# Kernel tuning notes

Hardware: AMD Instinct MI355X
Metric: run time of the kernel (lower is better)

The kernel has to match this reference:

```python
import jax, jax.numpy as jnp
import numpy as np

B, T, F = 16, 1024, 512       # batch, time, input_dim
G, V, D = 2, 320, 128         # num_groups, num_vars, var_dim (quantized_dim // G)
TAU = 2.0                     # max_temp * decay**0 at num_updates=0
EPS = 1e-7


def setup_inputs() -> dict:
    key = jax.random.key(0)
    kx, kw, kc, kg = jax.random.split(key, 4)
    x = jax.random.normal(kx, (B, T, F), dtype=jnp.float32)
    w_proj = jax.random.normal(kw, (G * V, F), dtype=jnp.float32)  # NormalLinear: std=1
    b_proj = jnp.zeros((G * V,), dtype=jnp.float32)
    codebook = jax.random.uniform(kc, (1, G * V, D), dtype=jnp.float32)  # uniform init
    u = jax.random.uniform(kg, (B * T, G, V), dtype=jnp.float32, minval=1e-10, maxval=1.0)
    gumbel = -jnp.log(-jnp.log(u))
    return {"x": x, "w_proj": w_proj, "b_proj": b_proj, "codebook": codebook, "gumbel": gumbel}


def reference(x, w_proj, b_proj, codebook, gumbel):
    bsz, tsz, _ = x.shape
    # projection -> (B, T, G, V)
    logits = (jnp.einsum("btf,nf->btn", x, w_proj) + b_proj).reshape(bsz, tsz, G, V)

    # hard one-hot of argmax (float32), like scatter_
    k = jnp.argmax(logits, axis=-1)
    hard_x = jax.nn.one_hot(k, V, dtype=jnp.float32)  # (B, T, G, V)

    # code perplexity: mean over batch dim only, sum over (T, G)
    hard_probs = hard_x.mean(axis=0)  # (T, G, V)
    code_perplexity = jnp.exp(-jnp.sum(hard_probs * jnp.log(hard_probs + EPS), axis=-1)).sum()

    # prob perplexity: softmax over codes, mean over all tokens, sum over groups
    flat_logits = logits.reshape(bsz * tsz, G, V)
    avg_probs = jax.nn.softmax(flat_logits, axis=-1).mean(axis=0)  # (G, V)
    prob_perplexity = jnp.exp(-jnp.sum(avg_probs * jnp.log(avg_probs + EPS), axis=-1)).sum()

    # gumbel-softmax, hard=True with straight-through estimator (training path)
    y_soft = jax.nn.softmax((flat_logits + gumbel) / TAU, axis=-1)  # (N, G, V)
    idx = jnp.argmax(y_soft, axis=-1)
    y_hard = jax.nn.one_hot(idx, V, dtype=y_soft.dtype)
    y = y_hard + y_soft - jax.lax.stop_gradient(y_soft)  # (N, G, V)

    # broadcast-multiply + sum over codes == grouped gather/matmul against codebook
    cb_gvd = codebook.reshape(G, V, D)
    quantized = jnp.einsum("ngv,gvd->ngd", y, cb_gvd).reshape(bsz, tsz, G * D)
    return quantized, code_perplexity, prob_perplexity
```

## Files before the change

kernel.cpp:

```cpp
#include <hip/hip_runtime.h>
#include <math.h>

#define B_   16
#define T_   1024
#define F_   512
#define G_   2
#define V_   320
#define D_   128
#define N_   (B_ * T_)
#define GV   (G_ * V_)
#define EPS_ 1e-7f

#define ROWS    64
#define THREADS 512
#define NBLK    (N_ / ROWS)
#define CHK     32
#define NCH     (F_ / CHK)
#define NCC     (3 * NCH)

#define BOFF  0
#define AOFF  40960
#define BUFSZ 45056
#define LDSZ  (2 * BUFSZ)

typedef _Float16 half8 __attribute__((ext_vector_type(8)));
typedef _Float16 half4 __attribute__((ext_vector_type(4)));
typedef float f32x16 __attribute__((ext_vector_type(16)));

#define CNTW      (T_ * G_ * (V_ / 2))
#define WS_COUNTS 0
#define WS_AVG    CNTW
#define WS_ENT    (WS_AVG + NBLK * GV)
#define WS_WH     (WS_ENT + T_ * G_)
#define WS_WL     (WS_WH + (GV * F_ / 2))
#define WS_AVGRED (WS_WL + (GV * F_ / 2))

__global__ __launch_bounds__(512) void k_conv_w(
    const float* __restrict__ w, _Float16* __restrict__ wh, _Float16* __restrict__ wl)
{
  const int i = blockIdx.x * 512 + threadIdx.x;
  const float4 v = ((const float4*)w)[i];
  half4 h, l;
#pragma unroll
  for (int k = 0; k < 4; ++k) {
    const float vk = ((const float*)&v)[k];
    const _Float16 hk = (_Float16)vk;
    h[k] = hk;
    l[k] = (_Float16)((vk - (float)hk) * 2048.0f);
  }
  ((half4*)wh)[i] = h;
  ((half4*)wl)[i] = l;
}

__global__ __launch_bounds__(THREADS, 1) void k_fused(
    const float* __restrict__ x, const _Float16* __restrict__ wh,
    const _Float16* __restrict__ wl, const float* __restrict__ bias,
    const float* __restrict__ cb, const float* __restrict__ gum,
    float* __restrict__ out, unsigned* __restrict__ counts,
    float* __restrict__ avg_part)
{
  __shared__ __align__(16) unsigned char SB[LDSZ];
  const int tid = threadIdx.x;
  const int wv  = tid >> 6;
  const int ln  = tid & 63;
  const int lo  = ln & 31, hi = ln >> 5;
  const int wvm = wv >> 2, wvn = wv & 3;
  const int blk = blockIdx.x;
  const int n0  = blk * ROWS;

  f32x16 acc[5];
#pragma unroll
  for (int t = 0; t < 5; ++t)
#pragma unroll
    for (int i = 0; i < 16; ++i) acc[t][i] = 0.0f;

  const int arow = tid >> 3, asub = tid & 7;
  const int aq = asub >> 1, ah = asub & 1;
  const float4* x4f = (const float4*)x;

  int aaddr[2], baddr[5][2];
  {
    const int ar = wvm * 32 + lo;
#pragma unroll
    for (int ks = 0; ks < 2; ++ks)
      aaddr[ks] = AOFF + ar * 64 + (((2 * ks + hi) ^ ((ar >> 1) & 3)) << 4);
#pragma unroll
    for (int t = 0; t < 5; ++t) {
      const int bn = wvn * 160 + t * 32 + lo;
#pragma unroll
      for (int ks = 0; ks < 2; ++ks)
        baddr[t][ks] = BOFF + bn * 64 + (((2 * ks + hi) ^ ((bn >> 1) & 3)) << 4);
    }
  }

  half8 bpre[5];
  float4 xpre;

#pragma unroll
  for (int it = 0; it < 5; ++it) {
    const int s = tid + it * THREADS;
    const int n = s >> 2, q = s & 3;
    bpre[it] = ((const half8*)wh)[n * 64 + q];
  }
  xpre = x4f[(size_t)(n0 + arow) * (F_ / 4) + asub];
  {
#pragma unroll
    for (int it = 0; it < 5; ++it) {
      const int s = tid + it * THREADS;
      const int n = s >> 2, q = s & 3;
      *(half8*)(SB + BOFF + n * 64 + ((q ^ ((n >> 1) & 3)) << 4)) = bpre[it];
    }
    half4 a4;
#pragma unroll
    for (int k = 0; k < 4; ++k) {
      const float vk = ((const float*)&xpre)[k];
      const _Float16 hk = (_Float16)vk;
      a4[k] = (_Float16)((vk - (float)hk) * 2048.0f);
    }
    *(half4*)(SB + AOFF + arow * 64 + ((aq ^ ((arow >> 1) & 3)) << 4) + ah * 8) = a4;
  }
  {
#pragma unroll
    for (int it = 0; it < 5; ++it) {
      const int s = tid + it * THREADS;
      const int n = s >> 2, q = s & 3;
      bpre[it] = ((const half8*)wh)[n * 64 + 4 + q];
    }
    xpre = x4f[(size_t)(n0 + arow) * (F_ / 4) + 8 + asub];
  }
  __builtin_amdgcn_sched_barrier(0);
  asm volatile("s_waitcnt lgkmcnt(0)" ::: "memory");
  __builtin_amdgcn_s_barrier();
  __builtin_amdgcn_sched_barrier(0);

  for (int cc = 0; cc < NCC; ++cc) {
    const int p = cc & 1;
    unsigned char* curb = SB + p * BUFSZ;
    unsigned char* nxtb = SB + (p ^ 1) * BUFSZ;
    if (cc + 1 < NCC) {
      const bool limb_lo = (cc + 1 < NCH);
#pragma unroll
      for (int it = 0; it < 5; ++it) {
        const int s = tid + it * THREADS;
        const int n = s >> 2, q = s & 3;
        *(half8*)(nxtb + BOFF + n * 64 + ((q ^ ((n >> 1) & 3)) << 4)) = bpre[it];
      }
      half4 a4;
#pragma unroll
      for (int k = 0; k < 4; ++k) {
        const float vk = ((const float*)&xpre)[k];
        const _Float16 hk = (_Float16)vk;
        a4[k] = limb_lo ? (_Float16)((vk - (float)hk) * 2048.0f) : hk;
      }
      *(half4*)(nxtb + AOFF + arow * 64 + ((aq ^ ((arow >> 1) & 3)) << 4) + ah * 8) = a4;
    }
    if (cc + 2 < NCC) {
      const int c2 = cc + 2;
      const _Float16* bs = ((c2 >> 4) == 1) ? wl : wh;
      const int k08 = (c2 & 15) * 4;
#pragma unroll
      for (int it = 0; it < 5; ++it) {
        const int s = tid + it * THREADS;
        const int n = s >> 2, q = s & 3;
        bpre[it] = ((const half8*)bs)[n * 64 + k08 + q];
      }
      xpre = x4f[(size_t)(n0 + arow) * (F_ / 4) + (c2 & 15) * 8 + asub];
    }
#pragma unroll
    for (int ks = 0; ks < 2; ++ks) {
      const half8 af = *(const half8*)(curb + aaddr[ks]);
#pragma unroll
      for (int t = 0; t < 5; ++t) {
        const half8 bf = *(const half8*)(curb + baddr[t][ks]);
        acc[t] = __builtin_amdgcn_mfma_f32_32x32x16_f16(af, bf, acc[t], 0, 0, 0);
      }
    }
    if (cc == 2 * NCH - 1) {
#pragma unroll
      for (int t = 0; t < 5; ++t)
#pragma unroll
        for (int i = 0; i < 16; ++i) acc[t][i] *= (1.0f / 2048.0f);
    }
    __builtin_amdgcn_sched_barrier(0);
    asm volatile("s_waitcnt lgkmcnt(0)" ::: "memory");
    __builtin_amdgcn_s_barrier();
    __builtin_amdgcn_sched_barrier(0);
  }

  float bfrag[5];
#pragma unroll
  for (int t = 0; t < 5; ++t) bfrag[t] = bias[wvn * 160 + t * 32 + lo];

  float racc[G_][5];
#pragma unroll
  for (int g = 0; g < G_; ++g)
#pragma unroll
    for (int j = 0; j < 5; ++j) racc[g][j] = 0.f;

  float* LBUF = (float*)SB;

#pragma unroll
  for (int R = 0; R < 4; ++R) {
    if (wvm == (R >> 1)) {
#pragma unroll
      for (int t = 0; t < 5; ++t) {
        const int col = wvn * 160 + t * 32 + lo;
#pragma unroll
        for (int rr = 0; rr < 8; ++rr) {
          const int reg  = ((R & 1) << 3) + rr;
          const int lrow = (rr & 3) + ((rr >> 2) << 3) + (hi << 2);
          LBUF[lrow * GV + col] = acc[t][reg] + bfrag[t];
        }
      }
    }
    __syncthreads();
#pragma unroll
    for (int rr2 = 0; rr2 < 2; ++rr2) {
      const int lrow = wv * 2 + rr2;
      const int n = n0 + R * 16 + lrow;
#pragma unroll
      for (int g = 0; g < G_; ++g) {
        float L[5], GU[5];
#pragma unroll
        for (int j = 0; j < 5; ++j) {
          L[j]  = LBUF[lrow * GV + g * V_ + 64 * j + ln];
          GU[j] = gum[(size_t)n * GV + g * V_ + 64 * j + ln];
        }
        float m1 = L[0];         int a1 = ln;
        float m2 = L[0] + GU[0]; int a2 = ln;
#pragma unroll
        for (int j = 1; j < 5; ++j) {
          const int cix = 64 * j + ln;
          if (L[j] > m1) { m1 = L[j]; a1 = cix; }
          const float t2 = L[j] + GU[j];
          if (t2 > m2) { m2 = t2; a2 = cix; }
        }
        for (int off = 32; off; off >>= 1) {
          float om = __shfl_down(m1, off); int oa = __shfl_down(a1, off);
          if (om > m1 || (om == m1 && oa < a1)) { m1 = om; a1 = oa; }
          float om2 = __shfl_down(m2, off); int oa2 = __shfl_down(a2, off);
          if (om2 > m2 || (om2 == m2 && oa2 < a2)) { m2 = om2; a2 = oa2; }
        }
        m1 = __shfl(m1, 0); a1 = __shfl(a1, 0); a2 = __shfl(a2, 0);

        float e[5], s = 0.f;
#pragma unroll
        for (int j = 0; j < 5; ++j) { e[j] = expf(L[j] - m1); s += e[j]; }
        for (int off = 32; off; off >>= 1) s += __shfl_down(s, off);
        s = __shfl(s, 0);
        const float inv = 1.0f / s;
#pragma unroll
        for (int j = 0; j < 5; ++j) racc[g][j] += e[j] * inv;

        if (ln == 0) {
          const int t = n & (T_ - 1);
          atomicAdd(&counts[(t * G_ + g) * (V_ / 2) + (a1 >> 1)],
                    1u << ((a1 & 1) * 16));
        }
        const float2* cbr = (const float2*)(cb + (size_t)(g * V_ + a2) * D_);
        float2* op = (float2*)(out + (size_t)n * (G_ * D_) + g * D_);
        op[ln] = cbr[ln];
      }
    }
    __syncthreads();
  }

  float* la = (float*)SB;
#pragma unroll
  for (int g = 0; g < G_; ++g)
#pragma unroll
    for (int j = 0; j < 5; ++j)
      la[wv * GV + g * V_ + 64 * j + ln] = racc[g][j];
  __syncthreads();
  for (int cix = tid; cix < GV; cix += THREADS) {
    float s = 0.f;
#pragma unroll
    for (int v = 0; v < 8; ++v) s += la[v * GV + cix];
    avg_part[(size_t)blk * GV + cix] = s;
  }
}

__global__ __launch_bounds__(256) void k_post(
    const unsigned* __restrict__ counts, float* __restrict__ ent,
    const float* __restrict__ avg_part, float* __restrict__ avgred)
{
  const int b = blockIdx.x;
  const int lane = threadIdx.x & 63;
  if (b < (T_ * G_) / 4) {
    const int item = b * 4 + (threadIdx.x >> 6);
    const unsigned* c = counts + (size_t)item * (V_ / 2);
    float s = 0.f;
#pragma unroll
    for (int j = 0; j < 3; ++j) {
      const int wi = lane + 64 * j;
      if (wi < V_ / 2) {
        const unsigned wd = c[wi];
        const float h0 = (float)(wd & 0xffffu) * (1.0f / B_);
        const float h1 = (float)(wd >> 16) * (1.0f / B_);
        s += h0 * logf(h0 + EPS_) + h1 * logf(h1 + EPS_);
      }
    }
    for (int off = 32; off; off >>= 1) s += __shfl_down(s, off);
    if (lane == 0) ent[item] = expf(-s);
  } else {
    const int cix = (b - (T_ * G_) / 4) * 4 + (threadIdx.x >> 6);
    float s = 0.f;
    for (int bb = lane; bb < NBLK; bb += 64) s += avg_part[(size_t)bb * GV + cix];
    for (int off = 32; off; off >>= 1) s += __shfl_down(s, off);
    if (lane == 0) avgred[cix] = s;
  }
}

__global__ __launch_bounds__(GV) void k_final(
    const float* __restrict__ avgred, const float* __restrict__ ent,
    float* __restrict__ out2)
{
  __shared__ float sh[GV];
  __shared__ float shc[GV];
  const int tid = threadIdx.x;

  const float p = avgred[tid] * (1.0f / N_);
  sh[tid] = p * logf(p + EPS_);

  float cs = 0.f;
  for (int i = tid; i < T_ * G_; i += GV) cs += ent[i];
  shc[tid] = cs;
  __syncthreads();

  if (tid < 64) {
    float s0 = 0.f, s1 = 0.f, sc = 0.f;
    for (int j = tid; j < V_; j += 64) { s0 += sh[j]; s1 += sh[V_ + j]; }
    for (int j = tid; j < GV; j += 64) sc += shc[j];
    for (int off = 32; off; off >>= 1) {
      s0 += __shfl_down(s0, off);
      s1 += __shfl_down(s1, off);
      sc += __shfl_down(sc, off);
    }
    if (tid == 0) {
      out2[0] = sc;
      out2[1] = expf(-s0) + expf(-s1);
    }
  }
}

extern "C" void kernel_launch(void* const* d_in, const int* in_sizes, int n_in,
                              void* d_out, int out_size, void* d_ws, size_t ws_size,
                              hipStream_t stream) {
  const float* x   = (const float*)d_in[0];
  const float* w   = (const float*)d_in[1];
  const float* b   = (const float*)d_in[2];
  const float* cb  = (const float*)d_in[3];
  const float* gum = (const float*)d_in[4];
  float* out = (float*)d_out;
  float* ws  = (float*)d_ws;

  unsigned* counts = (unsigned*)(ws + WS_COUNTS);
  float* avgp   = ws + WS_AVG;
  float* ent    = ws + WS_ENT;
  _Float16* whp = (_Float16*)(ws + WS_WH);
  _Float16* wlp = (_Float16*)(ws + WS_WL);
  float* avgred = ws + WS_AVGRED;

  hipMemsetAsync(counts, 0, (size_t)CNTW * sizeof(unsigned), stream);
  k_conv_w<<<(GV * F_ / 4) / 512, 512, 0, stream>>>(w, whp, wlp);
  k_fused<<<NBLK, THREADS, 0, stream>>>(x, whp, wlp, b, cb, gum, out, counts, avgp);
  k_post<<<(T_ * G_) / 4 + GV / 4, 256, 0, stream>>>(counts, ent, avgp, avgred);
  k_final<<<1, GV, 0, stream>>>(avgred, ent, out + (size_t)N_ * G_ * D_);
}
```

Baseline: 195.6 us.

## Pre-pack weights into MFMA fragment order and stream them with direct global-to-LDS loads

The weight conversion kernel now writes high and low fp16 limbs pre-tiled in MFMA fragment order. The fused kernel loads them straight into LDS with global_load_lds, so the register staging and swizzled LDS stores go away. Instead of three sequential passes over K (lo-limb A, lo-limb B, hi), each 16-wide K chunk now issues hi*hi, lo*hi and hi*lo MFMAs into two accumulators, and the loop count drops from 48 to 32. The launch bound is raised to allow 2 blocks per CU. This costs 80 extra accumulator VGPRs, and the 88KB LDS per block may still limit occupancy to one block.

```diff
diff --git a/kernel.cpp b/kernel.cpp
--- a/kernel.cpp
+++ b/kernel.cpp
@@ -14,9 +14,7 @@
 #define ROWS    64
 #define THREADS 512
 #define NBLK    (N_ / ROWS)
-#define CHK     32
-#define NCH     (F_ / CHK)
-#define NCC     (3 * NCH)
+#define NC      32
 
 #define BOFF  0
 #define AOFF  40960
@@ -24,40 +22,50 @@
 #define LDSZ  (2 * BUFSZ)
 
 typedef _Float16 half8 __attribute__((ext_vector_type(8)));
-typedef _Float16 half4 __attribute__((ext_vector_type(4)));
+typedef _Float16 half2_t __attribute__((ext_vector_type(2)));
 typedef float f32x16 __attribute__((ext_vector_type(16)));
+
+#define GLDS16(g, l)                                                           \
+  __builtin_amdgcn_global_load_lds(                                            \
+      (const __attribute__((address_space(1))) unsigned int*)(g),              \
+      (__attribute__((address_space(3))) unsigned int*)(l), 16, 0, 0)
 
 #define CNTW      (T_ * G_ * (V_ / 2))
 #define WS_COUNTS 0
 #define WS_AVG    CNTW
 #define WS_ENT    (WS_AVG + NBLK * GV)
-#define WS_WH     (WS_ENT + T_ * G_)
-#define WS_WL     (WS_WH + (GV * F_ / 2))
-#define WS_AVGRED (WS_WL + (GV * F_ / 2))
-
-__global__ __launch_bounds__(512) void k_conv_w(
-    const float* __restrict__ w, _Float16* __restrict__ wh, _Float16* __restrict__ wl)
+#define WS_WPK    (WS_ENT + T_ * G_)
+#define WS_AVGRED (WS_WPK + (GV * F_ * 2 / 2))
+
+__global__ __launch_bounds__(640) void k_conv_w(
+    const float* __restrict__ w, _Float16* __restrict__ wpk)
 {
-  const int i = blockIdx.x * 512 + threadIdx.x;
-  const float4 v = ((const float4*)w)[i];
-  half4 h, l;
-#pragma unroll
-  for (int k = 0; k < 4; ++k) {
-    const float vk = ((const float*)&v)[k];
-    const _Float16 hk = (_Float16)vk;
-    h[k] = hk;
-    l[k] = (_Float16)((vk - (float)hk) * 2048.0f);
-  }
-  ((half4*)wh)[i] = h;
-  ((half4*)wl)[i] = l;
-}
-
-__global__ __launch_bounds__(THREADS, 1) void k_fused(
-    const float* __restrict__ x, const _Float16* __restrict__ wh,
-    const _Float16* __restrict__ wl, const float* __restrict__ bias,
-    const float* __restrict__ cb, const float* __restrict__ gum,
-    float* __restrict__ out, unsigned* __restrict__ counts,
-    float* __restrict__ avg_part)
+  const int cl = blockIdx.x;
+  const int c = cl >> 1, limb = cl & 1;
+#pragma unroll
+  for (int it = 0; it < 2; ++it) {
+    const int t2 = threadIdx.x + it * 640;
+    const int n = t2 >> 6, ln = t2 & 63;
+    const int row = n * 32 + (ln & 31);
+    const int k0 = c * 16 + (ln >> 5) * 8;
+    const float4 v0 = *(const float4*)(w + (size_t)row * F_ + k0);
+    const float4 v1 = *(const float4*)(w + (size_t)row * F_ + k0 + 4);
+    half8 h;
+#pragma unroll
+    for (int k = 0; k < 8; ++k) {
+      const float vk = (k < 4) ? ((const float*)&v0)[k] : ((const float*)&v1)[k - 4];
+      const _Float16 hk = (_Float16)vk;
+      h[k] = limb ? (_Float16)((vk - (float)hk) * 2048.0f) : hk;
+    }
+    ((half8*)wpk)[((size_t)cl * 20 + n) * 64 + ln] = h;
+  }
+}
+
+__global__ __launch_bounds__(THREADS, 2) void k_fused(
+    const float* __restrict__ x, const _Float16* __restrict__ wpk,
+    const float* __restrict__ bias, const float* __restrict__ cb,
+    const float* __restrict__ gum, float* __restrict__ out,
+    unsigned* __restrict__ counts, float* __restrict__ avg_part)
 {
   __shared__ __align__(16) unsigned char SB[LDSZ];
   const int tid = threadIdx.x;
@@ -68,121 +76,84 @@
   const int blk = blockIdx.x;
   const int n0  = blk * ROWS;
 
-  f32x16 acc[5];
+  f32x16 ah_acc[5], al_acc[5];
 #pragma unroll
   for (int t = 0; t < 5; ++t)
 #pragma unroll
-    for (int i = 0; i < 16; ++i) acc[t][i] = 0.0f;
-
-  const int arow = tid >> 3, asub = tid & 7;
-  const int aq = asub >> 1, ah = asub & 1;
-  const float4* x4f = (const float4*)x;
-
-  int aaddr[2], baddr[5][2];
+    for (int i = 0; i < 16; ++i) { ah_acc[t][i] = 0.0f; al_acc[t][i] = 0.0f; }
+
+  const int arow = tid >> 3;
+  const int akp  = tid & 7;
+  const int awoff = (arow >> 5) * 1024 + (((akp >> 2) << 5) + (arow & 31)) * 16
+                  + (akp & 3) * 4;
+  const float2* x2 = (const float2*)x;
+  const size_t xrowbase = (size_t)(n0 + arow) * (F_ / 2) + akp;
+
+  const int aro_h = AOFF + 0 * 2048 + wvm * 1024 + ln * 16;
+  const int aro_l = AOFF + 1 * 2048 + wvm * 1024 + ln * 16;
+  int bro_h[5], bro_l[5];
+#pragma unroll
+  for (int t = 0; t < 5; ++t) {
+    bro_h[t] = BOFF + (0 * 20 + wvn * 5 + t) * 1024 + ln * 16;
+    bro_l[t] = BOFF + (1 * 20 + wvn * 5 + t) * 1024 + ln * 16;
+  }
+
   {
-    const int ar = wvm * 32 + lo;
-#pragma unroll
-    for (int ks = 0; ks < 2; ++ks)
-      aaddr[ks] = AOFF + ar * 64 + (((2 * ks + hi) ^ ((ar >> 1) & 3)) << 4);
-#pragma unroll
-    for (int t = 0; t < 5; ++t) {
-      const int bn = wvn * 160 + t * 32 + lo;
-#pragma unroll
-      for (int ks = 0; ks < 2; ++ks)
-        baddr[t][ks] = BOFF + bn * 64 + (((2 * ks + hi) ^ ((bn >> 1) & 3)) << 4);
-    }
-  }
-
-  half8 bpre[5];
-  float4 xpre;
-
-#pragma unroll
-  for (int it = 0; it < 5; ++it) {
-    const int s = tid + it * THREADS;
-    const int n = s >> 2, q = s & 3;
-    bpre[it] = ((const half8*)wh)[n * 64 + q];
-  }
-  xpre = x4f[(size_t)(n0 + arow) * (F_ / 4) + asub];
-  {
-#pragma unroll
-    for (int it = 0; it < 5; ++it) {
-      const int s = tid + it * THREADS;
-      const int n = s >> 2, q = s & 3;
-      *(half8*)(SB + BOFF + n * 64 + ((q ^ ((n >> 1) & 3)) << 4)) = bpre[it];
-    }
-    half4 a4;
-#pragma unroll
-    for (int k = 0; k < 4; ++k) {
-      const float vk = ((const float*)&xpre)[k];
-      const _Float16 hk = (_Float16)vk;
-      a4[k] = (_Float16)((vk - (float)hk) * 2048.0f);
-    }
-    *(half4*)(SB + AOFF + arow * 64 + ((aq ^ ((arow >> 1) & 3)) << 4) + ah * 8) = a4;
-  }
-  {
-#pragma unroll
-    for (int it = 0; it < 5; ++it) {
-      const int s = tid + it * THREADS;
-      const int n = s >> 2, q = s & 3;
-      bpre[it] = ((const half8*)wh)[n * 64 + 4 + q];
-    }
-    xpre = x4f[(size_t)(n0 + arow) * (F_ / 4) + 8 + asub];
+    const float2 xv = x2[xrowbase + 0 * 8];
+#pragma unroll
+    for (int i = 0; i < 5; ++i) {
+      const int seg = wv * 5 + i;
+      GLDS16(wpk + ((size_t)(0 * 40 + seg) * 64 + ln) * 8, SB + BOFF + seg * 1024);
+    }
+    half2_t hh, hl;
+#pragma unroll
+    for (int k = 0; k < 2; ++k) {
+      const float f = k ? xv.y : xv.x;
+      const _Float16 h = (_Float16)f;
+      hh[k] = h; hl[k] = (_Float16)((f - (float)h) * 2048.0f);
+    }
+    *(half2_t*)(SB + AOFF + awoff) = hh;
+    *(half2_t*)(SB + AOFF + 2048 + awoff) = hl;
   }
   __builtin_amdgcn_sched_barrier(0);
-  asm volatile("s_waitcnt lgkmcnt(0)" ::: "memory");
+  asm volatile("s_waitcnt vmcnt(0) lgkmcnt(0)" ::: "memory");
   __builtin_amdgcn_s_barrier();
   __builtin_amdgcn_sched_barrier(0);
 
-  for (int cc = 0; cc < NCC; ++cc) {
-    const int p = cc & 1;
-    unsigned char* curb = SB + p * BUFSZ;
-    unsigned char* nxtb = SB + (p ^ 1) * BUFSZ;
-    if (cc + 1 < NCC) {
-      const bool limb_lo = (cc + 1 < NCH);
-#pragma unroll
-      for (int it = 0; it < 5; ++it) {
-        const int s = tid + it * THREADS;
-        const int n = s >> 2, q = s & 3;
-        *(half8*)(nxtb + BOFF + n * 64 + ((q ^ ((n >> 1) & 3)) << 4)) = bpre[it];
-      }
-      half4 a4;
-#pragma unroll
-      for (int k = 0; k < 4; ++k) {
-        const float vk = ((const float*)&xpre)[k];
-        const _Float16 hk = (_Float16)vk;
-        a4[k] = limb_lo ? (_Float16)((vk - (float)hk) * 2048.0f) : hk;
-      }
-      *(half4*)(nxtb + AOFF + arow * 64 + ((aq ^ ((arow >> 1) & 3)) << 4) + ah * 8) = a4;
-    }
-    if (cc + 2 < NCC) {
-      const int c2 = cc + 2;
-      const _Float16* bs = ((c2 >> 4) == 1) ? wl : wh;
-      const int k08 = (c2 & 15) * 4;
-#pragma unroll
-      for (int it = 0; it < 5; ++it) {
-        const int s = tid + it * THREADS;
-        const int n = s >> 2, q = s & 3;
-        bpre[it] = ((const half8*)bs)[n * 64 + k08 + q];
-      }
-      xpre = x4f[(size_t)(n0 + arow) * (F_ / 4) + (c2 & 15) * 8 + asub];
-    }
-#pragma unroll
-    for (int ks = 0; ks < 2; ++ks) {
-      const half8 af = *(const half8*)(curb + aaddr[ks]);
-#pragma unroll
-      for (int t = 0; t < 5; ++t) {
-        const half8 bf = *(const half8*)(curb + baddr[t][ks]);
-        acc[t] = __builtin_amdgcn_mfma_f32_32x32x16_f16(af, bf, acc[t], 0, 0, 0);
-      }
-    }
-    if (cc == 2 * NCH - 1) {
-#pragma unroll
-      for (int t = 0; t < 5; ++t)
-#pragma unroll
-        for (int i = 0; i < 16; ++i) acc[t][i] *= (1.0f / 2048.0f);
+  for (int cc = 0; cc < NC; ++cc) {
+    unsigned char* curb = SB + (cc & 1) * BUFSZ;
+    unsigned char* nxtb = SB + ((cc & 1) ^ 1) * BUFSZ;
+    if (cc + 1 < NC) {
+      const int c1 = cc + 1;
+      const float2 xv = x2[xrowbase + c1 * 8];
+#pragma unroll
+      for (int i = 0; i < 5; ++i) {
+        const int seg = wv * 5 + i;
+        GLDS16(wpk + ((size_t)(c1 * 40 + seg) * 64 + ln) * 8,
+               nxtb + BOFF + seg * 1024);
+      }
+      half2_t hh, hl;
+#pragma unroll
+      for (int k = 0; k < 2; ++k) {
+        const float f = k ? xv.y : xv.x;
+        const _Float16 h = (_Float16)f;
+        hh[k] = h; hl[k] = (_Float16)((f - (float)h) * 2048.0f);
+      }
+      *(half2_t*)(nxtb + AOFF + awoff) = hh;
+      *(half2_t*)(nxtb + AOFF + 2048 + awoff) = hl;
+    }
+    const half8 ah = *(const half8*)(curb + aro_h);
+    const half8 al = *(const half8*)(curb + aro_l);
+#pragma unroll
+    for (int t = 0; t < 5; ++t) {
+      const half8 bh = *(const half8*)(curb + bro_h[t]);
+      const half8 bl = *(const half8*)(curb + bro_l[t]);
+      ah_acc[t] = __builtin_amdgcn_mfma_f32_32x32x16_f16(ah, bh, ah_acc[t], 0, 0, 0);
+      al_acc[t] = __builtin_amdgcn_mfma_f32_32x32x16_f16(al, bh, al_acc[t], 0, 0, 0);
+      al_acc[t] = __builtin_amdgcn_mfma_f32_32x32x16_f16(ah, bl, al_acc[t], 0, 0, 0);
     }
     __builtin_amdgcn_sched_barrier(0);
-    asm volatile("s_waitcnt lgkmcnt(0)" ::: "memory");
+    asm volatile("s_waitcnt vmcnt(0) lgkmcnt(0)" ::: "memory");
     __builtin_amdgcn_s_barrier();
     __builtin_amdgcn_sched_barrier(0);
   }
@@ -209,7 +180,8 @@
         for (int rr = 0; rr < 8; ++rr) {
           const int reg  = ((R & 1) << 3) + rr;
           const int lrow = (rr & 3) + ((rr >> 2) << 3) + (hi << 2);
-          LBUF[lrow * GV + col] = acc[t][reg] + bfrag[t];
+          LBUF[lrow * GV + col] =
+              ah_acc[t][reg] + al_acc[t][reg] * (1.0f / 2048.0f) + bfrag[t];
         }
       }
     }
@@ -357,13 +329,12 @@
   unsigned* counts = (unsigned*)(ws + WS_COUNTS);
   float* avgp   = ws + WS_AVG;
   float* ent    = ws + WS_ENT;
-  _Float16* whp = (_Float16*)(ws + WS_WH);
-  _Float16* wlp = (_Float16*)(ws + WS_WL);
+  _Float16* wpk = (_Float16*)(ws + WS_WPK);
   float* avgred = ws + WS_AVGRED;
 
   hipMemsetAsync(counts, 0, (size_t)CNTW * sizeof(unsigned), stream);
-  k_conv_w<<<(GV * F_ / 4) / 512, 512, 0, stream>>>(w, whp, wlp);
-  k_fused<<<NBLK, THREADS, 0, stream>>>(x, whp, wlp, b, cb, gum, out, counts, avgp);
+  k_conv_w<<<64, 640, 0, stream>>>(w, wpk);
+  k_fused<<<NBLK, THREADS, 0, stream>>>(x, wpk, b, cb, gum, out, counts, avgp);
   k_post<<<(T_ * G_) / 4 + GV / 4, 256, 0, stream>>>(counts, ent, avgp, avgred);
   k_final<<<1, GV, 0, stream>>>(avgred, ent, out + (size_t)N_ * G_ * D_);
 }
```

After: 188.6 us. -3.6%, faster.
